# Kernel optimization log

Hardware: AMD Instinct MI355X
Metric: run time of the kernel (lower is better)

The kernel has to match this reference:

```python
import jax, jax.numpy as jnp
import numpy as np

EPS = 1e-7
STRIDE = 1
PAD = 3


def _mantissa_map(v):
    # (|v|+eps) * 2^(-floor(log2(|v|+eps))) - 1  -> mantissa-1 in [0,1)
    a = jnp.abs(v) + EPS
    base = a * jnp.exp2(-jnp.floor(jnp.log2(a))) - 1.0
    # piecewise: >=0.5 -> (1+base)/2, else 1+base  (values in [0.75, 1.5))
    return jnp.where(base >= 0.5, (1.0 + base) * 0.5, 1.0 + base)


def _unfold(x, kH, kW, stride, pad, Ho, Wo):
    # im2col matching torch.nn.Unfold ordering (kernel position index = i*kW + j)
    xp = jnp.pad(x, ((0, 0), (0, 0), (pad, pad), (pad, pad)))
    cols = [xp[:, :, i:i + stride * Ho:stride, j:j + stride * Wo:stride]
            for i in range(kH) for j in range(kW)]
    return jnp.stack(cols, axis=-1)  # (B, C, Ho, Wo, kH*kW)


def setup_inputs() -> dict:
    key = jax.random.key(0)
    k1, k2 = jax.random.split(key)
    x = jax.random.normal(k1, (4, 192, 56, 56), dtype=jnp.float32)
    weight = jax.random.normal(k2, (192, 1, 7, 7), dtype=jnp.float32) * 0.1
    return {"x": x, "weight": weight}


def reference(x, weight):
    B, C, H, W = x.shape
    _, _, kH, kW = weight.shape
    Ho = (H + 2 * PAD - kH) // STRIDE + 1
    Wo = (W + 2 * PAD - kW) // STRIDE + 1
    KK = kH * kW

    # mantissa factors
    m2 = _mantissa_map(weight).reshape(C, KK)[None, :, None, None, :]  # (1,C,1,1,KK)
    m1 = _unfold(_mantissa_map(x), kH, kW, STRIDE, PAD, Ho, Wo)        # (B,C,Ho,Wo,KK)
    # zeros come only from unfold's zero padding; map them to 1 (then 0 after -1)
    m1 = jnp.where(m1 == 0.0, 1.0, m1) - 1.0
    m2 = m2 - 1.0

    factor = (m1 + m2 + 1.0) / ((m1 + 1.0) * (m2 + 1.0))
    factor = jnp.where(jnp.isfinite(factor), factor, 1.0)

    q_x = _unfold(x, kH, kW, STRIDE, PAD, Ho, Wo)          # (B,C,Ho,Wo,KK)
    w = weight.reshape(C, KK)[None, :, None, None, :]       # (1,C,1,1,KK)
    q_y = jnp.sum(factor * (q_x * w), axis=-1)              # (B,C,Ho,Wo)
    return q_y.astype(jnp.float32)
```

## Files before the change

kernel.cpp:

```cpp
#include <hip/hip_runtime.h>

typedef float v2f __attribute__((ext_vector_type(2)));
typedef float v4f __attribute__((ext_vector_type(4)));

#define EPS 1e-7f

__device__ __forceinline__ float mant_map(float v) {
    float a = fabsf(v) + EPS;
    unsigned int bi = __float_as_uint(a);
    float m = __uint_as_float((bi & 0x007FFFFFu) | 0x3F800000u);
    return (m >= 1.5f) ? 0.5f * m : m;
}

__global__ __launch_bounds__(128, 3) void wconv_kernel(const float* __restrict__ x,
                                                       const float* __restrict__ w,
                                                       float* __restrict__ out) {
    __shared__ v2f sp[34][64];
    __shared__ v2f swt[49];

    const int lx = threadIdx.x;
    const int ty = threadIdx.y;
    const int tid = ty * 32 + lx;
    const int c = blockIdx.x;
    const int b = blockIdx.y;
    const int tz = blockIdx.z;

    const int y0 = 28 * tz;
    const int g0 = (tz == 0) ? 0 : 25;
    const int l0 = (tz == 0) ? 3 : 0;
    const int z0 = (tz == 0) ? 0 : 31;

    const long plane = (long)(b * 192 + c) * 3136;
    const float* xp = x + plane;

    if (tid < 49) {
        float wv = w[c * 49 + tid];
        float M2 = mant_map(wv);
        float B = wv / M2;
        swt[tid] = (v2f){B, B * (M2 - 1.0f)};
    }

    for (int t = tid; t < 192; t += 128)
        ((v2f*)sp)[z0 * 64 + t] = (v2f){0.f, 0.f};
    for (int t = tid; t < 248; t += 128) {
        int r = l0 + (t >> 3), k = t & 7;
        int col = (k < 3) ? k : 56 + k;
        sp[r][col] = (v2f){0.f, 0.f};
    }

    for (int t = tid; t < 434; t += 128) {
        int r = t / 14, q4 = t % 14;
        v4f u4 = *(const v4f*)(xp + (g0 + r) * 56 + q4 * 4);
        v2f* dst = &sp[l0 + r][3 + q4 * 4];
        dst[0] = (v2f){u4.x, u4.x * __builtin_amdgcn_rcpf(mant_map(u4.x))};
        dst[1] = (v2f){u4.y, u4.y * __builtin_amdgcn_rcpf(mant_map(u4.y))};
        dst[2] = (v2f){u4.z, u4.z * __builtin_amdgcn_rcpf(mant_map(u4.z))};
        dst[3] = (v2f){u4.w, u4.w * __builtin_amdgcn_rcpf(mant_map(u4.w))};
    }
    __syncthreads();

    if (lx < 28) {
        const int x0 = lx * 2;
        const int rb = ty * 7;

        v2f a0[7], a1[7];
        #pragma unroll
        for (int r = 0; r < 7; ++r) { a0[r] = (v2f){0.f, 0.f}; a1[r] = (v2f){0.f, 0.f}; }

        #pragma unroll
        for (int ir = 0; ir < 13; ++ir) {
            const v4f* q = (const v4f*)&sp[rb + ir][x0];
            v4f q0 = q[0], q1 = q[1], q2 = q[2], q3 = q[3];
            v2f p[8] = {{q0.x, q0.y}, {q0.z, q0.w}, {q1.x, q1.y}, {q1.z, q1.w},
                        {q2.x, q2.y}, {q2.z, q2.w}, {q3.x, q3.y}, {q3.z, q3.w}};
            #pragma unroll
            for (int ry = 0; ry < 7; ++ry) {
                const int i = ir - ry;
                if (i >= 0 && i <= 6) {
                    #pragma unroll
                    for (int j = 0; j < 7; ++j) {
                        v2f wc = swt[i * 7 + j];
                        a0[ry] += p[j] * wc;
                        a1[ry] += p[j + 1] * wc;
                    }
                }
            }
        }

        #pragma unroll
        for (int ry = 0; ry < 7; ++ry) {
            float2 o = make_float2(a0[ry].x + a0[ry].y, a1[ry].x + a1[ry].y);
            *(float2*)&out[plane + (y0 + rb + ry) * 56 + x0] = o;
        }
    }
}

extern "C" void kernel_launch(void* const* d_in, const int* in_sizes, int n_in,
                              void* d_out, int out_size, void* d_ws, size_t ws_size,
                              hipStream_t stream) {
    const float* x = (const float*)d_in[0];
    const float* w = (const float*)d_in[1];
    float* out = (float*)d_out;

    hipLaunchKernelGGL(wconv_kernel, dim3(192, 4, 2), dim3(32, 4), 0, stream, x, w, out);
}
```

Baseline: 69.48 us.

## Compute four output columns per thread with vectorized weight loads

Each thread now computes 4 adjacent output columns instead of 2, so one 10-element LDS row load is reused across more outputs. Weights are stored as padded 16-float rows so a tap row can be fetched with v4 loads. The block shrinks from 128 to 64 threads (16x4) with matching launch bounds, and outputs are written with 128-bit stores. The trade-off is more registers per thread (28 v2f accumulators) and fewer threads per block, which may lower occupancy and latency hiding; the LDS staging loops also take more iterations per thread.

```diff
diff --git a/kernel.cpp b/kernel.cpp
--- a/kernel.cpp
+++ b/kernel.cpp
@@ -12,15 +12,15 @@
     return (m >= 1.5f) ? 0.5f * m : m;
 }
 
-__global__ __launch_bounds__(128, 3) void wconv_kernel(const float* __restrict__ x,
-                                                       const float* __restrict__ w,
-                                                       float* __restrict__ out) {
+__global__ __launch_bounds__(64, 2) void wconv_kernel(const float* __restrict__ x,
+                                                      const float* __restrict__ w,
+                                                      float* __restrict__ out) {
     __shared__ v2f sp[34][64];
-    __shared__ v2f swt[49];
+    __shared__ float swt[7][16];
 
     const int lx = threadIdx.x;
     const int ty = threadIdx.y;
-    const int tid = ty * 32 + lx;
+    const int tid = ty * 16 + lx;
     const int c = blockIdx.x;
     const int b = blockIdx.y;
     const int tz = blockIdx.z;
@@ -37,18 +37,24 @@
         float wv = w[c * 49 + tid];
         float M2 = mant_map(wv);
         float B = wv / M2;
-        swt[tid] = (v2f){B, B * (M2 - 1.0f)};
+        int i = tid / 7, j = tid - 7 * i;
+        swt[i][2 * j] = B;
+        swt[i][2 * j + 1] = B * (M2 - 1.0f);
+    } else if (tid < 56) {
+        int i = tid - 49;
+        swt[i][14] = 0.0f;
+        swt[i][15] = 0.0f;
     }
 
-    for (int t = tid; t < 192; t += 128)
+    for (int t = tid; t < 192; t += 64)
         ((v2f*)sp)[z0 * 64 + t] = (v2f){0.f, 0.f};
-    for (int t = tid; t < 248; t += 128) {
+    for (int t = tid; t < 248; t += 64) {
         int r = l0 + (t >> 3), k = t & 7;
         int col = (k < 3) ? k : 56 + k;
         sp[r][col] = (v2f){0.f, 0.f};
     }
 
-    for (int t = tid; t < 434; t += 128) {
+    for (int t = tid; t < 434; t += 64) {
         int r = t / 14, q4 = t % 14;
         v4f u4 = *(const v4f*)(xp + (g0 + r) * 56 + q4 * 4);
         v2f* dst = &sp[l0 + r][3 + q4 * 4];
@@ -59,38 +65,46 @@
     }
     __syncthreads();
 
-    if (lx < 28) {
-        const int x0 = lx * 2;
+    if (lx < 14) {
+        const int x0 = lx * 4;
         const int rb = ty * 7;
 
-        v2f a0[7], a1[7];
+        v2f acc[4][7];
         #pragma unroll
-        for (int r = 0; r < 7; ++r) { a0[r] = (v2f){0.f, 0.f}; a1[r] = (v2f){0.f, 0.f}; }
+        for (int c4 = 0; c4 < 4; ++c4)
+            #pragma unroll
+            for (int r = 0; r < 7; ++r) acc[c4][r] = (v2f){0.f, 0.f};
 
         #pragma unroll
         for (int ir = 0; ir < 13; ++ir) {
             const v4f* q = (const v4f*)&sp[rb + ir][x0];
-            v4f q0 = q[0], q1 = q[1], q2 = q[2], q3 = q[3];
-            v2f p[8] = {{q0.x, q0.y}, {q0.z, q0.w}, {q1.x, q1.y}, {q1.z, q1.w},
-                        {q2.x, q2.y}, {q2.z, q2.w}, {q3.x, q3.y}, {q3.z, q3.w}};
+            v4f q0 = q[0], q1 = q[1], q2 = q[2], q3 = q[3], q4 = q[4];
+            v2f p[10] = {{q0.x, q0.y}, {q0.z, q0.w}, {q1.x, q1.y}, {q1.z, q1.w},
+                         {q2.x, q2.y}, {q2.z, q2.w}, {q3.x, q3.y}, {q3.z, q3.w},
+                         {q4.x, q4.y}, {q4.z, q4.w}};
             #pragma unroll
             for (int ry = 0; ry < 7; ++ry) {
                 const int i = ir - ry;
                 if (i >= 0 && i <= 6) {
+                    const v4f* wr = (const v4f*)swt[i];
+                    v4f w0 = wr[0], w1 = wr[1], w2 = wr[2], w3 = wr[3];
+                    v2f wt2[7] = {{w0.x, w0.y}, {w0.z, w0.w}, {w1.x, w1.y},
+                                  {w1.z, w1.w}, {w2.x, w2.y}, {w2.z, w2.w},
+                                  {w3.x, w3.y}};
                     #pragma unroll
-                    for (int j = 0; j < 7; ++j) {
-                        v2f wc = swt[i * 7 + j];
-                        a0[ry] += p[j] * wc;
-                        a1[ry] += p[j + 1] * wc;
-                    }
+                    for (int c4 = 0; c4 < 4; ++c4)
+                        #pragma unroll
+                        for (int j = 0; j < 7; ++j)
+                            acc[c4][ry] += p[c4 + j] * wt2[j];
                 }
             }
         }
 
         #pragma unroll
         for (int ry = 0; ry < 7; ++ry) {
-            float2 o = make_float2(a0[ry].x + a0[ry].y, a1[ry].x + a1[ry].y);
-            *(float2*)&out[plane + (y0 + rb + ry) * 56 + x0] = o;
+            v4f o = {acc[0][ry].x + acc[0][ry].y, acc[1][ry].x + acc[1][ry].y,
+                     acc[2][ry].x + acc[2][ry].y, acc[3][ry].x + acc[3][ry].y};
+            *(v4f*)&out[plane + (y0 + rb + ry) * 56 + x0] = o;
         }
     }
 }
@@ -102,5 +116,5 @@
     const float* w = (const float*)d_in[1];
     float* out = (float*)d_out;
 
-    hipLaunchKernelGGL(wconv_kernel, dim3(192, 4, 2), dim3(32, 4), 0, stream, x, w, out);
+    hipLaunchKernelGGL(wconv_kernel, dim3(192, 4, 2), dim3(16, 4), 0, stream, x, w, out);
 }
```

Result: slower. 71.93 us (+3.5%).
